# Kernel optimization log

Hardware: AMD Instinct MI355X
Metric: run time of the kernel (lower is better)

## Reference

```python
import jax, jax.numpy as jnp
import numpy as np

N_NODES = 100000
N_EDGES = 1600000
D = 128          # gnn_input_size == gnn_hidden_size
N_LAYERS = 7
N_GRAPHS = 64
N_CLASSES = 10
SNN_IN, SNN_H = 512, 1024
SNN_BETA = 0.85


def setup_inputs() -> dict:
    key = jax.random.key(0)
    ks = jax.random.split(key, 16)
    s = 0.05  # keep activations tame through 7 relu layers
    return {
        "snn_x": jax.random.normal(ks[0], (N_GRAPHS, SNN_IN), jnp.float32),
        "x": jax.random.normal(ks[1], (N_NODES, D), jnp.float32),
        "edge_index": jax.random.randint(ks[2], (2, N_EDGES), 0, N_NODES, jnp.int64),
        "batch": jnp.sort(jax.random.randint(ks[3], (N_NODES,), 0, N_GRAPHS, jnp.int64)),
        "snn_w1": jax.random.normal(ks[4], (SNN_IN, SNN_H), jnp.float32) * s,
        "snn_b1": jax.random.normal(ks[5], (SNN_H,), jnp.float32) * s,
        "snn_w2": jax.random.normal(ks[6], (SNN_H, N_CLASSES), jnp.float32) * s,
        "snn_b2": jax.random.normal(ks[7], (N_CLASSES,), jnp.float32) * s,
        "conv_wrel": jax.random.normal(ks[8], (N_LAYERS, D, D), jnp.float32) * s,
        "conv_wroot": jax.random.normal(ks[9], (N_LAYERS, D, D), jnp.float32) * s,
        "conv_brel": jax.random.normal(ks[10], (N_LAYERS, D), jnp.float32) * s,
        "lin_w": jax.random.normal(ks[11], (D, N_CLASSES), jnp.float32) * s,
        "lin_b": jax.random.normal(ks[12], (N_CLASSES,), jnp.float32) * s,
        "fuse_w": jax.random.normal(ks[13], (2 * N_CLASSES, N_CLASSES), jnp.float32) * s,
        "fuse_b": jax.random.normal(ks[14], (N_CLASSES,), jnp.float32) * s,
    }


def reference(snn_x, x, edge_index, batch,
              snn_w1, snn_b1, snn_w2, snn_b2,
              conv_wrel, conv_wroot, conv_brel,
              lin_w, lin_b, fuse_w, fuse_b):
    n = x.shape[0]
    src, dst = edge_index[0], edge_index[1]
    h = x
    for i in range(conv_wrel.shape[0]):
        agg = jax.ops.segment_sum(h[src], dst, num_segments=n)  # gather + scatter-add
        h = jax.nn.relu(agg @ conv_wrel[i] + conv_brel[i] + h @ conv_wroot[i])
    # global_mean_pool over batch segments
    sums = jax.ops.segment_sum(h, batch, num_segments=N_GRAPHS)
    cnts = jax.ops.segment_sum(jnp.ones((n,), h.dtype), batch, num_segments=N_GRAPHS)
    pooled = sums / jnp.maximum(cnts, 1.0)[:, None]
    gnn_logits = pooled @ lin_w + lin_b
    # SNN branch
    snn_h = jax.nn.relu(snn_x @ snn_w1 + snn_b1)
    snn_logits = SNN_BETA * (snn_h @ snn_w2 + snn_b2)
    # fusion
    fused = jnp.concatenate([snn_logits, gnn_logits], axis=-1)
    return fused @ fuse_w + fuse_b
```

## Files before the change

kernel.cpp:

```cpp
#include <hip/hip_runtime.h>
#include <hip/hip_bf16.h>

#define N_NODES 100000
#define N_EDGES 1600000
#define DIM     128
#define N_LAYERS 7
#define N_GRAPHS 64
#define SNN_IN  512
#define SNN_HID 1024
#define NCLS    10
#define M_PAD   100096
#define MBLK    782
#define NBK     782
#define SORT_CHUNK 4096
#define SORT_NCH   391
#define XPAIRS  (N_NODES * 64)
#define HPAIRS  (M_PAD * 64)
#define WELEMS  (N_LAYERS * DIM * 256)
#define AGG_BLOCKS 2048
#define AGG_WAVES  (AGG_BLOCKS * 4)
#define NQUAD   (N_NODES / 4)
#define POOL_NB 782
#define SS_PAD  2000384

typedef __attribute__((ext_vector_type(8))) short short8;
typedef __attribute__((ext_vector_type(4))) float f32x4;

__device__ __forceinline__ unsigned int f2bf(float f) {
    unsigned int u = __float_as_uint(f);
    return (u + 0x7fffu + ((u >> 16) & 1u)) >> 16;
}
__device__ __forceinline__ float bf2f(unsigned short b) {
    return __uint_as_float(((unsigned int)b) << 16);
}
__device__ __forceinline__ void acc_pair(unsigned int u, float& lo, float& hi) {
    lo += __uint_as_float(u << 16);
    hi += __uint_as_float(u & 0xffff0000u);
}

__global__ void k_convert(const float* __restrict__ x, const float* __restrict__ wrel,
                          const float* __restrict__ wroot, unsigned int* __restrict__ h,
                          unsigned short* __restrict__ Wt,
                          float* __restrict__ pooled, int* __restrict__ counts) {
    int i = blockIdx.x * blockDim.x + threadIdx.x;
    if (i < N_GRAPHS * 128) pooled[i] = 0.f;
    if (i >= N_GRAPHS * 128 && i < N_GRAPHS * 129) counts[i - N_GRAPHS * 128] = 0;
    if (i < XPAIRS) {
        float2 v = ((const float2*)x)[i];
        h[i] = f2bf(v.x) | (f2bf(v.y) << 16);
    } else if (i < HPAIRS) {
        h[i] = 0u;
    } else {
        int idx = i - HPAIRS;
        if (idx < WELEMS) {
            int l = idx >> 15, rem = idx & 32767, n = rem >> 8, k = rem & 255;
            float v = (k < 128) ? wrel[l * 16384 + k * 128 + n]
                                : wroot[l * 16384 + (k - 128) * 128 + n];
            Wt[idx] = (unsigned short)f2bf(v);
        }
    }
}

__global__ __launch_bounds__(256) void k_histA(const int* __restrict__ dst,
                                               int* __restrict__ chunk_hist) {
    __shared__ int hist[NBK];
    int b = blockIdx.x, t = threadIdx.x;
    int e0 = b * SORT_CHUNK;
    int e1 = e0 + SORT_CHUNK; if (e1 > N_EDGES) e1 = N_EDGES;
    for (int i = t; i < NBK; i += 256) hist[i] = 0;
    __syncthreads();
    for (int e = e0 + t; e < e1; e += 256) atomicAdd(&hist[dst[e] >> 7], 1);
    __syncthreads();
    for (int i = t; i < NBK; i += 256) chunk_hist[b * NBK + i] = hist[i];
}

__global__ __launch_bounds__(64) void k_colscan(int* __restrict__ chunk_hist,
                                                int* __restrict__ btot) {
    int b = blockIdx.x;
    int lane = threadIdx.x;
    const int C = (SORT_NCH + 63) / 64;
    int vals[C]; int sum = 0;
    #pragma unroll
    for (int j = 0; j < C; j++) {
        int c = lane * C + j;
        vals[j] = (c < SORT_NCH) ? chunk_hist[c * NBK + b] : 0;
        sum += vals[j];
    }
    int s = sum;
    #pragma unroll
    for (int o = 1; o < 64; o <<= 1) { int t = __shfl_up(s, o); if (lane >= o) s += t; }
    if (lane == 63) btot[b] = s;
    int run = s - sum;
    #pragma unroll
    for (int j = 0; j < C; j++) {
        int c = lane * C + j;
        if (c < SORT_NCH) chunk_hist[c * NBK + b] = run;
        run += vals[j];
    }
}

__global__ __launch_bounds__(256) void k_bscan(const int* __restrict__ btot,
                                               int* __restrict__ bucket_base) {
    __shared__ int wsum[4];
    int tid = threadIdx.x, lane = tid & 63, wid = tid >> 6;
    int i0 = tid * 4;
    int v[4]; int sum = 0;
    #pragma unroll
    for (int j = 0; j < 4; j++) { int i = i0 + j; v[j] = (i < NBK) ? btot[i] : 0; sum += v[j]; }
    int s = sum;
    #pragma unroll
    for (int o = 1; o < 64; o <<= 1) { int t = __shfl_up(s, o); if (lane >= o) s += t; }
    if (lane == 63) wsum[wid] = s;
    __syncthreads();
    if (tid == 0) {
        int acc = 0;
        #pragma unroll
        for (int w = 0; w < 4; w++) { acc += wsum[w]; wsum[w] = acc; }
    }
    __syncthreads();
    int prefix = s - sum + (wid ? wsum[wid - 1] : 0);
    #pragma unroll
    for (int j = 0; j < 4; j++) { int i = i0 + j; if (i < NBK) bucket_base[i] = prefix; prefix += v[j]; }
}

__global__ __launch_bounds__(256) void k_scatterA(const int* __restrict__ src,
                                                  const int* __restrict__ dst,
                                                  const int* __restrict__ chunk_hist,
                                                  const int* __restrict__ bucket_base,
                                                  unsigned int* __restrict__ pairs) {
    __shared__ int lcur[NBK];
    int b = blockIdx.x, t = threadIdx.x;
    int e0 = b * SORT_CHUNK;
    int e1 = e0 + SORT_CHUNK; if (e1 > N_EDGES) e1 = N_EDGES;
    for (int i = t; i < NBK; i += 256) lcur[i] = chunk_hist[b * NBK + i] + bucket_base[i];
    __syncthreads();
    for (int e = e0 + t; e < e1; e += 256) {
        int d = dst[e];
        int bk = d >> 7;
        int pos = atomicAdd(&lcur[bk], 1);
        pairs[pos] = (unsigned int)src[e] | ((unsigned int)(d & 127) << 17);
    }
}

__global__ __launch_bounds__(256) void k_bucketB(const unsigned int* __restrict__ pairs,
                                                 const int* __restrict__ bucket_base,
                                                 const int* __restrict__ btot,
                                                 int* __restrict__ row_off,
                                                 int* __restrict__ ndeg,
                                                 int* __restrict__ sorted_src) {
    __shared__ int lcnt[128];
    __shared__ int loff[128];
    int b = blockIdx.x, t = threadIdx.x;
    int node0 = b << 7;
    int nn = N_NODES - node0; if (nn > 128) nn = 128;
    int base = bucket_base[b];
    int end  = base + btot[b];
    int pbase = ((base + 3) & ~3) + 512 * b;
    if (t < 128) lcnt[t] = 0;
    __syncthreads();
    for (int i = base + t; i < end; i += 256) atomicAdd(&lcnt[pairs[i] >> 17], 1);
    __syncthreads();
    if (t < 64) {
        int v0 = (lcnt[2 * t] + 3) & ~3, v1 = (lcnt[2 * t + 1] + 3) & ~3;
        int s = v0 + v1, ps = s;
        #pragma unroll
        for (int o = 1; o < 64; o <<= 1) { int u = __shfl_up(ps, o); if (t >= o) ps += u; }
        int excl = ps - s;
        loff[2 * t] = excl; loff[2 * t + 1] = excl + v0;
    }
    __syncthreads();
    if (t < nn) {
        int d = lcnt[t];
        row_off[node0 + t] = pbase + loff[t];
        ndeg[node0 + t] = d;
        int pad = (d + 3) & ~3;
        for (int k = d; k < pad; k++) sorted_src[pbase + loff[t] + k] = N_NODES;
    }
    __syncthreads();
    if (t < 128) lcnt[t] = 0;
    __syncthreads();
    for (int i = base + t; i < end; i += 256) {
        unsigned int p = pairs[i];
        int l = p >> 17;
        int pos = atomicAdd(&lcnt[l], 1);
        sorted_src[pbase + loff[l] + pos] = (int)(p & 0x1FFFFu);
    }
}

#define GATH(d0, d1, d2, d3, s) \
    d0 = *(const uint4*)(hbl + (size_t)(((unsigned)(s).x) << 8)); \
    d1 = *(const uint4*)(hbl + (size_t)(((unsigned)(s).y) << 8)); \
    d2 = *(const uint4*)(hbl + (size_t)(((unsigned)(s).z) << 8)); \
    d3 = *(const uint4*)(hbl + (size_t)(((unsigned)(s).w) << 8));
#define ACC4(r0, r1, r2, r3) \
    acc_pair((r0).x, a[0], a[1]); acc_pair((r0).y, a[2], a[3]); \
    acc_pair((r0).z, a[4], a[5]); acc_pair((r0).w, a[6], a[7]); \
    acc_pair((r1).x, a[0], a[1]); acc_pair((r1).y, a[2], a[3]); \
    acc_pair((r1).z, a[4], a[5]); acc_pair((r1).w, a[6], a[7]); \
    acc_pair((r2).x, a[0], a[1]); acc_pair((r2).y, a[2], a[3]); \
    acc_pair((r2).z, a[4], a[5]); acc_pair((r2).w, a[6], a[7]); \
    acc_pair((r3).x, a[0], a[1]); acc_pair((r3).y, a[2], a[3]); \
    acc_pair((r3).z, a[4], a[5]); acc_pair((r3).w, a[6], a[7]);

__global__ __launch_bounds__(256) void k_agg(const char* __restrict__ hb,
                                             const int* __restrict__ row_off,
                                             const int* __restrict__ ndeg,
                                             const int4* __restrict__ sorted4,
                                             uint4* __restrict__ agg4) {
    int gw = blockIdx.x * 4 + (threadIdx.x >> 6);
    int lane = threadIdx.x & 63;
    int sub = lane >> 4, li = lane & 15;
    const char* hbl = hb + li * 16;
    for (int quad = gw; quad < NQUAD; quad += AGG_WAVES) {
        int node = quad * 4 + sub;
        int beg = row_off[node] >> 2;
        int nit = (ndeg[node] + 3) >> 2;
        float a[8] = {0.f, 0.f, 0.f, 0.f, 0.f, 0.f, 0.f, 0.f};
        if (nit > 0) {
            int4 sa = sorted4[beg];
            int4 sb = sorted4[beg + 1];
            uint4 A0, A1, A2, A3, B0, B1, B2, B3;
            GATH(A0, A1, A2, A3, sa);
            int it = 0;
            for (; it + 2 < nit; it += 2) {
                GATH(B0, B1, B2, B3, sb);
                sa = sorted4[beg + it + 2];
                ACC4(A0, A1, A2, A3);
                GATH(A0, A1, A2, A3, sa);
                sb = sorted4[beg + it + 3];
                ACC4(B0, B1, B2, B3);
            }
            if (it + 1 < nit) {
                GATH(B0, B1, B2, B3, sb);
                ACC4(A0, A1, A2, A3);
                ACC4(B0, B1, B2, B3);
            } else {
                ACC4(A0, A1, A2, A3);
            }
        }
        uint4 o;
        o.x = f2bf(a[0]) | (f2bf(a[1]) << 16);
        o.y = f2bf(a[2]) | (f2bf(a[3]) << 16);
        o.z = f2bf(a[4]) | (f2bf(a[5]) << 16);
        o.w = f2bf(a[6]) | (f2bf(a[7]) << 16);
        agg4[(size_t)node * 16 + li] = o;
    }
}

__global__ __launch_bounds__(256) void k_gemm(const unsigned short* __restrict__ Ag,
                                              const unsigned short* __restrict__ H,
                                              const unsigned short* __restrict__ Wt,
                                              const float* __restrict__ bias,
                                              unsigned short* __restrict__ Hout) {
    __shared__ unsigned short Es[64 * 144];
    int tid = threadIdx.x;
    int lane = tid & 63, wid = tid >> 6;
    int wr = (wid >> 1) * 64, wc = (wid & 1) * 64;
    int row0 = blockIdx.x * 128;
    f32x4 acc[4][4] = {};

    int ksub = (lane >> 4) * 8;
    const unsigned short* Aga = Ag + (size_t)(row0 + wr + (lane & 15)) * 128 + ksub;
    const unsigned short* Ha  = H  + (size_t)(row0 + wr + (lane & 15)) * 128 + ksub;
    const unsigned short* Bb  = Wt + (size_t)(wc + (lane & 15)) * 256 + ksub;

    auto load_frags = [&](short8* a, short8* b, int s) {
        const unsigned short* ab = (s < 4 ? Aga : Ha) + (s & 3) * 32;
        #pragma unroll
        for (int mi = 0; mi < 4; mi++) a[mi] = *(const short8*)(ab + mi * 16 * 128);
        const unsigned short* bp = Bb + s * 32;
        #pragma unroll
        for (int ni = 0; ni < 4; ni++) b[ni] = *(const short8*)(bp + ni * 16 * 256);
    };
    auto do_mfma = [&](short8* a, short8* b) {
        #pragma unroll
        for (int mi = 0; mi < 4; mi++)
            #pragma unroll
            for (int ni = 0; ni < 4; ni++)
                acc[mi][ni] = __builtin_amdgcn_mfma_f32_16x16x32_bf16(a[mi], b[ni], acc[mi][ni], 0, 0, 0);
    };

    short8 a0[4], b0[4], a1[4], b1[4];
    load_frags(a0, b0, 0);
    #pragma unroll
    for (int s = 0; s < 8; s += 2) {
        load_frags(a1, b1, s + 1);
        do_mfma(a0, b0);
        if (s + 2 < 8) load_frags(a0, b0, s + 2);
        do_mfma(a1, b1);
    }

    int cb = wc + (lane & 15);
    int rs = (lane >> 4) * 4;
    #pragma unroll
    for (int p = 0; p < 2; ++p) {
        __syncthreads();
        if (wr == 64 * p) {
            #pragma unroll
            for (int ni = 0; ni < 4; ni++) {
                int col = cb + ni * 16;
                float bn = bias[col];
                #pragma unroll
                for (int mi = 0; mi < 4; mi++) {
                    int rloc = mi * 16 + rs;
                    #pragma unroll
                    for (int rr = 0; rr < 4; rr++) {
                        float v = acc[mi][ni][rr] + bn;
                        v = v > 0.f ? v : 0.f;
                        if (row0 + 64 * p + rloc + rr >= N_NODES) v = 0.f;
                        Es[(rloc + rr) * 144 + col] = (unsigned short)f2bf(v);
                    }
                }
            }
        }
        __syncthreads();
        int rloc = tid >> 2;
        int c4 = (tid & 3) * 4;
        uint4* gd = (uint4*)(Hout + (size_t)(row0 + 64 * p + rloc) * 128);
        const uint4* es = (const uint4*)(Es + (size_t)rloc * 144);
        #pragma unroll
        for (int j = 0; j < 4; j++) gd[c4 + j] = es[c4 + j];
    }
}

__global__ __launch_bounds__(256) void k_pool_snn(const unsigned short* __restrict__ h,
                                                  const int* __restrict__ batch,
                                                  float* __restrict__ pooled,
                                                  int* __restrict__ counts,
                                                  const float* __restrict__ x,
                                                  const float* __restrict__ w1,
                                                  const float* __restrict__ b1,
                                                  float* __restrict__ snn_out) {
    if (blockIdx.x < POOL_NB) {
        __shared__ int bsh[128];
        int start = blockIdx.x * 128;
        int t = threadIdx.x & 127;
        int half = threadIdx.x >> 7;
        if (half == 0) {
            int end = start + 128; if (end > N_NODES) end = N_NODES;
            int nn = end - start;
            if (t < nn) bsh[t] = batch[start + t];
        }
        __syncthreads();
        if (half == 1) {
            int end = start + 128; if (end > N_NODES) end = N_NODES;
            int nn = end - start;
            float acc = 0.f; int cur = -1, cnt = 0;
            for (int i = 0; i < nn; i++) {
                int g = bsh[i];
                if (g != cur) {
                    if (cur >= 0) { atomicAdd(&pooled[cur * 128 + t], acc); if (t == 0) atomicAdd(&counts[cur], cnt); }
                    cur = g; acc = 0.f; cnt = 0;
                }
                acc += bf2f(h[(size_t)(start + i) * 128 + t]);
                cnt++;
            }
            if (cur >= 0) { atomicAdd(&pooled[cur * 128 + t], acc); if (t == 0) atomicAdd(&counts[cur], cnt); }
        }
    } else {
        int m = blockIdx.x - POOL_NB;
        __shared__ float xs[SNN_IN];
        int tid = threadIdx.x;
        for (int i = tid; i < SNN_IN; i += 256) xs[i] = x[m * SNN_IN + i];
        __syncthreads();
        float a0 = 0.f, a1 = 0.f, a2 = 0.f, a3 = 0.f;
        for (int k = 0; k < SNN_IN; k++) {
            float xv = xs[k];
            const float* wr = w1 + (size_t)k * SNN_HID + tid;
            a0 += xv * wr[0]; a1 += xv * wr[256]; a2 += xv * wr[512]; a3 += xv * wr[768];
        }
        float v;
        v = a0 + b1[tid];       snn_out[m * SNN_HID + tid]       = v > 0.f ? v : 0.f;
        v = a1 + b1[tid + 256]; snn_out[m * SNN_HID + tid + 256] = v > 0.f ? v : 0.f;
        v = a2 + b1[tid + 512]; snn_out[m * SNN_HID + tid + 512] = v > 0.f ? v : 0.f;
        v = a3 + b1[tid + 768]; snn_out[m * SNN_HID + tid + 768] = v > 0.f ? v : 0.f;
    }
}

__global__ __launch_bounds__(64) void k_head(const float* __restrict__ pooled, const int* __restrict__ counts,
                                             const float* __restrict__ lin_w, const float* __restrict__ lin_b,
                                             const float* __restrict__ snn_h, const float* __restrict__ w2,
                                             const float* __restrict__ b2, const float* __restrict__ fuse_w,
                                             const float* __restrict__ fuse_b, float* __restrict__ out) {
    int m = blockIdx.x, lane = threadIdx.x;
    __shared__ float sm[20];
    float cnt = (float)(counts[m] > 0 ? counts[m] : 1);
    float p0 = pooled[m * 128 + lane] / cnt;
    float p1 = pooled[m * 128 + 64 + lane] / cnt;
    for (int c = 0; c < NCLS; c++) {
        float v = p0 * lin_w[lane * 10 + c] + p1 * lin_w[(lane + 64) * 10 + c];
        #pragma unroll
        for (int o = 32; o > 0; o >>= 1) v += __shfl_down(v, o);
        if (lane == 0) sm[10 + c] = v + lin_b[c];
    }
    for (int c = 0; c < NCLS; c++) {
        float v = 0.f;
        #pragma unroll
        for (int j = 0; j < 16; j++) {
            int k = lane + j * 64;
            v += snn_h[m * SNN_HID + k] * w2[k * 10 + c];
        }
        #pragma unroll
        for (int o = 32; o > 0; o >>= 1) v += __shfl_down(v, o);
        if (lane == 0) sm[c] = 0.85f * (v + b2[c]);
    }
    __syncthreads();
    if (lane < NCLS) {
        float o = fuse_b[lane];
        #pragma unroll
        for (int j = 0; j < 20; j++) o += sm[j] * fuse_w[j * 10 + lane];
        out[m * 10 + lane] = o;
    }
}

extern "C" void kernel_launch(void* const* d_in, const int* in_sizes, int n_in,
                              void* d_out, int out_size, void* d_ws, size_t ws_size,
                              hipStream_t stream) {
    const float* snn_x  = (const float*)d_in[0];
    const float* x      = (const float*)d_in[1];
    const int*   ei     = (const int*)d_in[2];
    const int*   batch  = (const int*)d_in[3];
    const float* w1     = (const float*)d_in[4];
    const float* b1     = (const float*)d_in[5];
    const float* w2     = (const float*)d_in[6];
    const float* b2     = (const float*)d_in[7];
    const float* wrel   = (const float*)d_in[8];
    const float* wroot  = (const float*)d_in[9];
    const float* brel   = (const float*)d_in[10];
    const float* lin_w  = (const float*)d_in[11];
    const float* lin_b  = (const float*)d_in[12];
    const float* fuse_w = (const float*)d_in[13];
    const float* fuse_b = (const float*)d_in[14];
    const int* srcv = ei;
    const int* dstv = ei + N_EDGES;

    char* ws = (char*)d_ws;
    size_t off = 0;
    auto alloc = [&](size_t b) { char* p = ws + off; off = (off + b + 255) & ~(size_t)255; return p; };
    unsigned short* h0   = (unsigned short*)alloc((size_t)M_PAD * 128 * 2);
    unsigned short* h1   = (unsigned short*)alloc((size_t)M_PAD * 128 * 2);
    unsigned short* agg  = (unsigned short*)alloc((size_t)M_PAD * 128 * 2);
    unsigned short* Wt   = (unsigned short*)alloc((size_t)N_LAYERS * 128 * 256 * 2);
    int* sorted_src = (int*)alloc((size_t)SS_PAD * 4 + 16);
    unsigned int* pairs = (unsigned int*)alloc((size_t)N_EDGES * 4);
    int* chunk_hist = (int*)alloc((size_t)SORT_NCH * NBK * 4);
    int* row_off    = (int*)alloc((size_t)(N_NODES + 1) * 4);
    int* ndeg       = (int*)alloc((size_t)N_NODES * 4);
    int* btot       = (int*)alloc((size_t)NBK * 4);
    int* bucket_base= (int*)alloc((size_t)NBK * 4);
    float* pooled   = (float*)alloc((size_t)N_GRAPHS * 128 * 4);
    int* counts     = (int*)alloc((size_t)N_GRAPHS * 4);
    float* snn_h    = (float*)alloc((size_t)N_GRAPHS * SNN_HID * 4);

    k_histA<<<SORT_NCH, 256, 0, stream>>>(dstv, chunk_hist);
    k_colscan<<<NBK, 64, 0, stream>>>(chunk_hist, btot);
    k_bscan<<<1, 256, 0, stream>>>(btot, bucket_base);
    k_scatterA<<<SORT_NCH, 256, 0, stream>>>(srcv, dstv, chunk_hist, bucket_base, pairs);
    k_bucketB<<<NBK, 256, 0, stream>>>(pairs, bucket_base, btot, row_off, ndeg, sorted_src);
    k_convert<<<(HPAIRS + WELEMS + 255) / 256, 256, 0, stream>>>(x, wrel, wroot, (unsigned int*)h0,
                                                                 Wt, pooled, counts);

    unsigned short* hc = h0;
    unsigned short* hn = h1;
    for (int l = 0; l < N_LAYERS; l++) {
        k_agg<<<AGG_BLOCKS, 256, 0, stream>>>((const char*)hc, row_off, ndeg,
                                              (const int4*)sorted_src, (uint4*)agg);
        k_gemm<<<MBLK, 256, 0, stream>>>(agg, hc, Wt + (size_t)l * 128 * 256, brel + l * 128, hn);
        unsigned short* t = hc; hc = hn; hn = t;
    }
    k_pool_snn<<<POOL_NB + N_GRAPHS, 256, 0, stream>>>(hc, batch, pooled, counts,
                                                       snn_x, w1, b1, snn_h);
    k_head<<<N_GRAPHS, 64, 0, stream>>>(pooled, counts, lin_w, lin_b, snn_h, w2, b2, fuse_w, fuse_b,
                                        (float*)d_out);
}
```

Before: 932.5 us.

## Sort nodes by degree so aggregation waves process similar-degree nodes

Adds a degree histogram, a reverse scan and a scatter pass that build a node permutation ordered by descending in-degree. The aggregation kernel now reads its node IDs through this permutation, so the four nodes that share a wave have similar neighbor counts. This is meant to cut idle lanes caused by degree imbalance inside a wave. In exchange it adds three small preprocessing kernels and an extra indirection, and it loses sequential locality on the row_off and ndeg reads and on the output writes.

New measurement: 1.226 ms. 1.31x slower.

```diff
diff --git a/kernel.cpp b/kernel.cpp
--- a/kernel.cpp
+++ b/kernel.cpp
@@ -22,6 +22,7 @@
 #define NQUAD   (N_NODES / 4)
 #define POOL_NB 782
 #define SS_PAD  2000384
+#define DEG_BINS 64
 
 typedef __attribute__((ext_vector_type(8))) short short8;
 typedef __attribute__((ext_vector_type(4))) float f32x4;
@@ -100,9 +101,11 @@
 }
 
 __global__ __launch_bounds__(256) void k_bscan(const int* __restrict__ btot,
-                                               int* __restrict__ bucket_base) {
+                                               int* __restrict__ bucket_base,
+                                               int* __restrict__ deg_hist) {
     __shared__ int wsum[4];
     int tid = threadIdx.x, lane = tid & 63, wid = tid >> 6;
+    if (tid < DEG_BINS) deg_hist[tid] = 0;
     int i0 = tid * 4;
     int v[4]; int sum = 0;
     #pragma unroll
@@ -187,6 +190,43 @@
     }
 }
 
+__global__ __launch_bounds__(256) void k_deghist(const int* __restrict__ ndeg,
+                                                 int* __restrict__ hist) {
+    __shared__ int lh[DEG_BINS];
+    int t = threadIdx.x;
+    if (t < DEG_BINS) lh[t] = 0;
+    __syncthreads();
+    int i = blockIdx.x * 256 + t;
+    if (i < N_NODES) {
+        int d = ndeg[i]; if (d > DEG_BINS - 1) d = DEG_BINS - 1;
+        atomicAdd(&lh[d], 1);
+    }
+    __syncthreads();
+    if (t < DEG_BINS && lh[t]) atomicAdd(&hist[t], lh[t]);
+}
+
+__global__ __launch_bounds__(64) void k_degscan(const int* __restrict__ hist,
+                                                int* __restrict__ cursor) {
+    int t = threadIdx.x;
+    int rd = DEG_BINS - 1 - t;
+    int v = hist[rd];
+    int s = v;
+    #pragma unroll
+    for (int o = 1; o < 64; o <<= 1) { int u = __shfl_up(s, o); if (t >= o) s += u; }
+    cursor[rd] = s - v;
+}
+
+__global__ __launch_bounds__(256) void k_degscatter(const int* __restrict__ ndeg,
+                                                    int* __restrict__ cursor,
+                                                    int* __restrict__ qnode) {
+    int i = blockIdx.x * 256 + threadIdx.x;
+    if (i < N_NODES) {
+        int d = ndeg[i]; if (d > DEG_BINS - 1) d = DEG_BINS - 1;
+        int pos = atomicAdd(&cursor[d], 1);
+        qnode[pos] = i;
+    }
+}
+
 #define GATH(d0, d1, d2, d3, s) \
     d0 = *(const uint4*)(hbl + (size_t)(((unsigned)(s).x) << 8)); \
     d1 = *(const uint4*)(hbl + (size_t)(((unsigned)(s).y) << 8)); \
@@ -206,13 +246,14 @@
                                              const int* __restrict__ row_off,
                                              const int* __restrict__ ndeg,
                                              const int4* __restrict__ sorted4,
+                                             const int* __restrict__ qnode,
                                              uint4* __restrict__ agg4) {
     int gw = blockIdx.x * 4 + (threadIdx.x >> 6);
     int lane = threadIdx.x & 63;
     int sub = lane >> 4, li = lane & 15;
     const char* hbl = hb + li * 16;
     for (int quad = gw; quad < NQUAD; quad += AGG_WAVES) {
-        int node = quad * 4 + sub;
+        int node = qnode[quad * 4 + sub];
         int beg = row_off[node] >> 2;
         int nit = (ndeg[node] + 3) >> 2;
         float a[8] = {0.f, 0.f, 0.f, 0.f, 0.f, 0.f, 0.f, 0.f};
@@ -446,6 +487,9 @@
     int* chunk_hist = (int*)alloc((size_t)SORT_NCH * NBK * 4);
     int* row_off    = (int*)alloc((size_t)(N_NODES + 1) * 4);
     int* ndeg       = (int*)alloc((size_t)N_NODES * 4);
+    int* qnode      = (int*)alloc((size_t)N_NODES * 4);
+    int* deg_hist   = (int*)alloc((size_t)DEG_BINS * 4);
+    int* deg_cursor = (int*)alloc((size_t)DEG_BINS * 4);
     int* btot       = (int*)alloc((size_t)NBK * 4);
     int* bucket_base= (int*)alloc((size_t)NBK * 4);
     float* pooled   = (float*)alloc((size_t)N_GRAPHS * 128 * 4);
@@ -454,9 +498,12 @@
 
     k_histA<<<SORT_NCH, 256, 0, stream>>>(dstv, chunk_hist);
     k_colscan<<<NBK, 64, 0, stream>>>(chunk_hist, btot);
-    k_bscan<<<1, 256, 0, stream>>>(btot, bucket_base);
+    k_bscan<<<1, 256, 0, stream>>>(btot, bucket_base, deg_hist);
     k_scatterA<<<SORT_NCH, 256, 0, stream>>>(srcv, dstv, chunk_hist, bucket_base, pairs);
     k_bucketB<<<NBK, 256, 0, stream>>>(pairs, bucket_base, btot, row_off, ndeg, sorted_src);
+    k_deghist<<<(N_NODES + 255) / 256, 256, 0, stream>>>(ndeg, deg_hist);
+    k_degscan<<<1, 64, 0, stream>>>(deg_hist, deg_cursor);
+    k_degscatter<<<(N_NODES + 255) / 256, 256, 0, stream>>>(ndeg, deg_cursor, qnode);
     k_convert<<<(HPAIRS + WELEMS + 255) / 256, 256, 0, stream>>>(x, wrel, wroot, (unsigned int*)h0,
                                                                  Wt, pooled, counts);
 
@@ -464,7 +511,7 @@
     unsigned short* hn = h1;
     for (int l = 0; l < N_LAYERS; l++) {
         k_agg<<<AGG_BLOCKS, 256, 0, stream>>>((const char*)hc, row_off, ndeg,
-                                              (const int4*)sorted_src, (uint4*)agg);
+                                              (const int4*)sorted_src, qnode, (uint4*)agg);
         k_gemm<<<MBLK, 256, 0, stream>>>(agg, hc, Wt + (size_t)l * 128 * 256, brel + l * 128, hn);
         unsigned short* t = hc; hc = hn; hn = t;
     }
```

## Fuse neighbor aggregation with GraphConv GEMM into one per-layer kernel

Applied to the files above, without the earlier changes.

Replaces the separate aggregation and GEMM kernels with one kernel per layer. Each wave gathers and sums the neighbor rows for 16 nodes in registers, packs the sums straight into MFMA A fragments, and overlaps the gather for the next 16-node group with the current group's matrix multiply. This removes the intermediate aggregate buffer's global write and read and one launch per layer. In exchange, each lane now walks a different node's edge list, so the gather loads are less coalesced and lanes diverge when node degrees differ. Output stores are also no longer staged through shared memory.

Measured after the change: 1.828 ms. +96.0%, slower.

```diff
diff --git a/kernel.cpp b/kernel.cpp
--- a/kernel.cpp
+++ b/kernel.cpp
@@ -17,14 +17,13 @@
 #define XPAIRS  (N_NODES * 64)
 #define HPAIRS  (M_PAD * 64)
 #define WELEMS  (N_LAYERS * DIM * 256)
-#define AGG_BLOCKS 2048
-#define AGG_WAVES  (AGG_BLOCKS * 4)
-#define NQUAD   (N_NODES / 4)
 #define POOL_NB 782
 #define SS_PAD  2000384
+#define NG_REAL 6250
 
 typedef __attribute__((ext_vector_type(8))) short short8;
 typedef __attribute__((ext_vector_type(4))) float f32x4;
+typedef __attribute__((ext_vector_type(4))) unsigned int u32x4;
 
 __device__ __forceinline__ unsigned int f2bf(float f) {
     unsigned int u = __float_as_uint(f);
@@ -187,139 +186,129 @@
     }
 }
 
-#define GATH(d0, d1, d2, d3, s) \
-    d0 = *(const uint4*)(hbl + (size_t)(((unsigned)(s).x) << 8)); \
-    d1 = *(const uint4*)(hbl + (size_t)(((unsigned)(s).y) << 8)); \
-    d2 = *(const uint4*)(hbl + (size_t)(((unsigned)(s).z) << 8)); \
-    d3 = *(const uint4*)(hbl + (size_t)(((unsigned)(s).w) << 8));
-#define ACC4(r0, r1, r2, r3) \
-    acc_pair((r0).x, a[0], a[1]); acc_pair((r0).y, a[2], a[3]); \
-    acc_pair((r0).z, a[4], a[5]); acc_pair((r0).w, a[6], a[7]); \
-    acc_pair((r1).x, a[0], a[1]); acc_pair((r1).y, a[2], a[3]); \
-    acc_pair((r1).z, a[4], a[5]); acc_pair((r1).w, a[6], a[7]); \
-    acc_pair((r2).x, a[0], a[1]); acc_pair((r2).y, a[2], a[3]); \
-    acc_pair((r2).z, a[4], a[5]); acc_pair((r2).w, a[6], a[7]); \
-    acc_pair((r3).x, a[0], a[1]); acc_pair((r3).y, a[2], a[3]); \
-    acc_pair((r3).z, a[4], a[5]); acc_pair((r3).w, a[6], a[7]);
-
-__global__ __launch_bounds__(256) void k_agg(const char* __restrict__ hb,
-                                             const int* __restrict__ row_off,
-                                             const int* __restrict__ ndeg,
-                                             const int4* __restrict__ sorted4,
-                                             uint4* __restrict__ agg4) {
-    int gw = blockIdx.x * 4 + (threadIdx.x >> 6);
-    int lane = threadIdx.x & 63;
-    int sub = lane >> 4, li = lane & 15;
-    const char* hbl = hb + li * 16;
-    for (int quad = gw; quad < NQUAD; quad += AGG_WAVES) {
-        int node = quad * 4 + sub;
-        int beg = row_off[node] >> 2;
-        int nit = (ndeg[node] + 3) >> 2;
-        float a[8] = {0.f, 0.f, 0.f, 0.f, 0.f, 0.f, 0.f, 0.f};
-        if (nit > 0) {
-            int4 sa = sorted4[beg];
-            int4 sb = sorted4[beg + 1];
+#define CONSUME(c0, c1, c2, c3) do { \
+    acc_pair((c0).x, ac[0],  ac[1]);  acc_pair((c0).y, ac[2],  ac[3]);  \
+    acc_pair((c0).z, ac[4],  ac[5]);  acc_pair((c0).w, ac[6],  ac[7]);  \
+    acc_pair((c1).x, ac[8],  ac[9]);  acc_pair((c1).y, ac[10], ac[11]); \
+    acc_pair((c1).z, ac[12], ac[13]); acc_pair((c1).w, ac[14], ac[15]); \
+    acc_pair((c2).x, ac[16], ac[17]); acc_pair((c2).y, ac[18], ac[19]); \
+    acc_pair((c2).z, ac[20], ac[21]); acc_pair((c2).w, ac[22], ac[23]); \
+    acc_pair((c3).x, ac[24], ac[25]); acc_pair((c3).y, ac[26], ac[27]); \
+    acc_pair((c3).z, ac[28], ac[29]); acc_pair((c3).w, ac[30], ac[31]); \
+} while (0)
+
+__global__ __launch_bounds__(256) void k_fused(const char* __restrict__ hb,
+                                               const int* __restrict__ row_off,
+                                               const int* __restrict__ ndeg,
+                                               const int* __restrict__ sorted_src,
+                                               const unsigned short* __restrict__ WtL,
+                                               const float* __restrict__ bias,
+                                               unsigned short* __restrict__ Hout) {
+    int tid = threadIdx.x, lane = tid & 63, wi = tid >> 6;
+    int l4 = lane & 15, hq = lane >> 4;
+    const char* hbl = hb + hq * 16;
+    const char* bb  = (const char*)WtL + 512 * l4 + 16 * hq;
+
+    int ga = blockIdx.x * 8 + wi * 2;
+    if (ga >= NG_REAL) return;
+    int gb = ga + 1;
+    bool hasB = gb < NG_REAL;
+
+    float ac[32];
+    int g_it = 0, g_nit = 0;
+    const int* g_ssp = sorted_src;
+
+    auto ginit = [&](int g) {
+        int node = (g << 4) + l4;
+        g_nit = ndeg[node];
+        g_ssp = sorted_src + row_off[node];
+        g_it = 0;
+        #pragma unroll
+        for (int i = 0; i < 32; i++) ac[i] = 0.f;
+    };
+
+    auto grest = [&]() {
+        while (__ballot(g_it < g_nit)) {
+            if (g_it < g_nit) {
+                int x = g_ssp[g_it];
+                const char* p = hbl + ((size_t)(unsigned)x << 8);
+                uint4 c0 = *(const uint4*)p;
+                uint4 c1 = *(const uint4*)(p + 64);
+                uint4 c2 = *(const uint4*)(p + 128);
+                uint4 c3 = *(const uint4*)(p + 192);
+                CONSUME(c0, c1, c2, c3);
+            }
+            g_it++;
+        }
+    };
+
+    short8 afr[4];
+    auto packfr = [&]() {
+        #pragma unroll
+        for (int c = 0; c < 4; c++) {
+            u32x4 t;
+            t[0] = f2bf(ac[8 * c + 0]) | (f2bf(ac[8 * c + 1]) << 16);
+            t[1] = f2bf(ac[8 * c + 2]) | (f2bf(ac[8 * c + 3]) << 16);
+            t[2] = f2bf(ac[8 * c + 4]) | (f2bf(ac[8 * c + 5]) << 16);
+            t[3] = f2bf(ac[8 * c + 6]) | (f2bf(ac[8 * c + 7]) << 16);
+            afr[c] = __builtin_bit_cast(short8, t);
+        }
+    };
+
+    auto ctile = [&](int crow) {
+        const char* hr = hb + (size_t)(crow + l4) * 256 + 16 * hq;
+        f32x4 acc4[8];
+        #pragma unroll
+        for (int ni = 0; ni < 8; ni++) acc4[ni] = (f32x4){0.f, 0.f, 0.f, 0.f};
+        #pragma unroll
+        for (int s = 0; s < 8; s++) {
+            bool v0 = g_it < g_nit, v1 = g_it + 1 < g_nit;
             uint4 A0, A1, A2, A3, B0, B1, B2, B3;
-            GATH(A0, A1, A2, A3, sa);
-            int it = 0;
-            for (; it + 2 < nit; it += 2) {
-                GATH(B0, B1, B2, B3, sb);
-                sa = sorted4[beg + it + 2];
-                ACC4(A0, A1, A2, A3);
-                GATH(A0, A1, A2, A3, sa);
-                sb = sorted4[beg + it + 3];
-                ACC4(B0, B1, B2, B3);
-            }
-            if (it + 1 < nit) {
-                GATH(B0, B1, B2, B3, sb);
-                ACC4(A0, A1, A2, A3);
-                ACC4(B0, B1, B2, B3);
-            } else {
-                ACC4(A0, A1, A2, A3);
-            }
-        }
-        uint4 o;
-        o.x = f2bf(a[0]) | (f2bf(a[1]) << 16);
-        o.y = f2bf(a[2]) | (f2bf(a[3]) << 16);
-        o.z = f2bf(a[4]) | (f2bf(a[5]) << 16);
-        o.w = f2bf(a[6]) | (f2bf(a[7]) << 16);
-        agg4[(size_t)node * 16 + li] = o;
-    }
-}
-
-__global__ __launch_bounds__(256) void k_gemm(const unsigned short* __restrict__ Ag,
-                                              const unsigned short* __restrict__ H,
-                                              const unsigned short* __restrict__ Wt,
-                                              const float* __restrict__ bias,
-                                              unsigned short* __restrict__ Hout) {
-    __shared__ unsigned short Es[64 * 144];
-    int tid = threadIdx.x;
-    int lane = tid & 63, wid = tid >> 6;
-    int wr = (wid >> 1) * 64, wc = (wid & 1) * 64;
-    int row0 = blockIdx.x * 128;
-    f32x4 acc[4][4] = {};
-
-    int ksub = (lane >> 4) * 8;
-    const unsigned short* Aga = Ag + (size_t)(row0 + wr + (lane & 15)) * 128 + ksub;
-    const unsigned short* Ha  = H  + (size_t)(row0 + wr + (lane & 15)) * 128 + ksub;
-    const unsigned short* Bb  = Wt + (size_t)(wc + (lane & 15)) * 256 + ksub;
-
-    auto load_frags = [&](short8* a, short8* b, int s) {
-        const unsigned short* ab = (s < 4 ? Aga : Ha) + (s & 3) * 32;
-        #pragma unroll
-        for (int mi = 0; mi < 4; mi++) a[mi] = *(const short8*)(ab + mi * 16 * 128);
-        const unsigned short* bp = Bb + s * 32;
-        #pragma unroll
-        for (int ni = 0; ni < 4; ni++) b[ni] = *(const short8*)(bp + ni * 16 * 256);
+            if (v0) {
+                int x = g_ssp[g_it];
+                const char* p = hbl + ((size_t)(unsigned)x << 8);
+                A0 = *(const uint4*)p;         A1 = *(const uint4*)(p + 64);
+                A2 = *(const uint4*)(p + 128); A3 = *(const uint4*)(p + 192);
+            }
+            if (v1) {
+                int x = g_ssp[g_it + 1];
+                const char* p = hbl + ((size_t)(unsigned)x << 8);
+                B0 = *(const uint4*)p;         B1 = *(const uint4*)(p + 64);
+                B2 = *(const uint4*)(p + 128); B3 = *(const uint4*)(p + 192);
+            }
+            g_it += 2;
+            short8 av = (s < 4) ? afr[s] : *(const short8*)(hr + 64 * (s - 4));
+            #pragma unroll
+            for (int ni = 0; ni < 8; ni++) {
+                short8 bv = *(const short8*)(bb + ni * 8192 + s * 64);
+                acc4[ni] = __builtin_amdgcn_mfma_f32_16x16x32_bf16(av, bv, acc4[ni], 0, 0, 0);
+            }
+            if (v0) CONSUME(A0, A1, A2, A3);
+            if (v1) CONSUME(B0, B1, B2, B3);
+        }
+        #pragma unroll
+        for (int ni = 0; ni < 8; ni++) {
+            float bn = bias[ni * 16 + l4];
+            #pragma unroll
+            for (int rr = 0; rr < 4; rr++) {
+                int row = crow + 4 * hq + rr;
+                float v = acc4[ni][rr] + bn;
+                v = v > 0.f ? v : 0.f;
+                Hout[(size_t)row * 128 + ni * 16 + l4] = (unsigned short)f2bf(v);
+            }
+        }
     };
-    auto do_mfma = [&](short8* a, short8* b) {
-        #pragma unroll
-        for (int mi = 0; mi < 4; mi++)
-            #pragma unroll
-            for (int ni = 0; ni < 4; ni++)
-                acc[mi][ni] = __builtin_amdgcn_mfma_f32_16x16x32_bf16(a[mi], b[ni], acc[mi][ni], 0, 0, 0);
-    };
-
-    short8 a0[4], b0[4], a1[4], b1[4];
-    load_frags(a0, b0, 0);
-    #pragma unroll
-    for (int s = 0; s < 8; s += 2) {
-        load_frags(a1, b1, s + 1);
-        do_mfma(a0, b0);
-        if (s + 2 < 8) load_frags(a0, b0, s + 2);
-        do_mfma(a1, b1);
-    }
-
-    int cb = wc + (lane & 15);
-    int rs = (lane >> 4) * 4;
-    #pragma unroll
-    for (int p = 0; p < 2; ++p) {
-        __syncthreads();
-        if (wr == 64 * p) {
-            #pragma unroll
-            for (int ni = 0; ni < 4; ni++) {
-                int col = cb + ni * 16;
-                float bn = bias[col];
-                #pragma unroll
-                for (int mi = 0; mi < 4; mi++) {
-                    int rloc = mi * 16 + rs;
-                    #pragma unroll
-                    for (int rr = 0; rr < 4; rr++) {
-                        float v = acc[mi][ni][rr] + bn;
-                        v = v > 0.f ? v : 0.f;
-                        if (row0 + 64 * p + rloc + rr >= N_NODES) v = 0.f;
-                        Es[(rloc + rr) * 144 + col] = (unsigned short)f2bf(v);
-                    }
-                }
-            }
-        }
-        __syncthreads();
-        int rloc = tid >> 2;
-        int c4 = (tid & 3) * 4;
-        uint4* gd = (uint4*)(Hout + (size_t)(row0 + 64 * p + rloc) * 128);
-        const uint4* es = (const uint4*)(Es + (size_t)rloc * 144);
-        #pragma unroll
-        for (int j = 0; j < 4; j++) gd[c4 + j] = es[c4 + j];
+
+    ginit(ga);
+    grest();
+    packfr();
+    if (hasB) ginit(gb); else { g_nit = 0; g_it = 0; }
+    ctile(ga << 4);
+    grest();
+    if (hasB) {
+        packfr();
+        g_nit = 0; g_it = 0;
+        ctile(gb << 4);
     }
 }
 
@@ -439,7 +428,6 @@
     auto alloc = [&](size_t b) { char* p = ws + off; off = (off + b + 255) & ~(size_t)255; return p; };
     unsigned short* h0   = (unsigned short*)alloc((size_t)M_PAD * 128 * 2);
     unsigned short* h1   = (unsigned short*)alloc((size_t)M_PAD * 128 * 2);
-    unsigned short* agg  = (unsigned short*)alloc((size_t)M_PAD * 128 * 2);
     unsigned short* Wt   = (unsigned short*)alloc((size_t)N_LAYERS * 128 * 256 * 2);
     int* sorted_src = (int*)alloc((size_t)SS_PAD * 4 + 16);
     unsigned int* pairs = (unsigned int*)alloc((size_t)N_EDGES * 4);
@@ -463,9 +451,8 @@
     unsigned short* hc = h0;
     unsigned short* hn = h1;
     for (int l = 0; l < N_LAYERS; l++) {
-        k_agg<<<AGG_BLOCKS, 256, 0, stream>>>((const char*)hc, row_off, ndeg,
-                                              (const int4*)sorted_src, (uint4*)agg);
-        k_gemm<<<MBLK, 256, 0, stream>>>(agg, hc, Wt + (size_t)l * 128 * 256, brel + l * 128, hn);
+        k_fused<<<MBLK, 256, 0, stream>>>((const char*)hc, row_off, ndeg, sorted_src,
+                                          Wt + (size_t)l * 128 * 256, brel + l * 128, hn);
         unsigned short* t = hc; hc = hn; hn = t;
     }
     k_pool_snn<<<POOL_NB + N_GRAPHS, 256, 0, stream>>>(hc, batch, pooled, counts,
```

## Stage GEMM A tiles through swizzled LDS with async global_load_lds double buffering

Applied to the files above, without the earlier changes.

The GEMM used to load A fragments (aggregated and root features) straight from global memory into registers, with each wave re-reading its rows. It now stages 128x64 A tiles into LDS with the async global_load_lds path, using an XOR swizzle and double buffering across four k-steps, then reads the fragments from LDS. B fragments still come straight from global memory. This should cut duplicate global traffic and overlap loads with MFMA work, at the cost of more block-wide barriers and 32KB of LDS per block, which may lower occupancy.

After: 865.3 us. 1.08x faster.

```diff
diff --git a/kernel.cpp b/kernel.cpp
--- a/kernel.cpp
+++ b/kernel.cpp
@@ -22,6 +22,9 @@
 #define NQUAD   (N_NODES / 4)
 #define POOL_NB 782
 #define SS_PAD  2000384
+
+#define AS1 __attribute__((address_space(1)))
+#define AS3 __attribute__((address_space(3)))
 
 typedef __attribute__((ext_vector_type(8))) short short8;
 typedef __attribute__((ext_vector_type(4))) float f32x4;
@@ -252,46 +255,67 @@
                                               const unsigned short* __restrict__ Wt,
                                               const float* __restrict__ bias,
                                               unsigned short* __restrict__ Hout) {
-    __shared__ unsigned short Es[64 * 144];
+    __shared__ char smem[32768];
     int tid = threadIdx.x;
     int lane = tid & 63, wid = tid >> 6;
     int wr = (wid >> 1) * 64, wc = (wid & 1) * 64;
     int row0 = blockIdx.x * 128;
+    int l4 = lane & 15, hq = lane >> 4;
     f32x4 acc[4][4] = {};
 
-    int ksub = (lane >> 4) * 8;
-    const unsigned short* Aga = Ag + (size_t)(row0 + wr + (lane & 15)) * 128 + ksub;
-    const unsigned short* Ha  = H  + (size_t)(row0 + wr + (lane & 15)) * 128 + ksub;
-    const unsigned short* Bb  = Wt + (size_t)(wc + (lane & 15)) * 256 + ksub;
-
-    auto load_frags = [&](short8* a, short8* b, int s) {
-        const unsigned short* ab = (s < 4 ? Aga : Ha) + (s & 3) * 32;
-        #pragma unroll
-        for (int mi = 0; mi < 4; mi++) a[mi] = *(const short8*)(ab + mi * 16 * 128);
-        const unsigned short* bp = Bb + s * 32;
-        #pragma unroll
-        for (int ni = 0; ni < 4; ni++) b[ni] = *(const short8*)(bp + ni * 16 * 256);
+    int srow = tid >> 3, scc = tid & 7;
+    const unsigned short* bb = Wt + (size_t)(wc + l4) * 256 + hq * 8;
+
+    auto stage = [&](int buf, int kt) {
+        const unsigned short* P = (kt < 2) ? Ag : H;
+        int kbase = (kt & 1) * 64;
+        #pragma unroll
+        for (int j = 0; j < 4; j++) {
+            int row = srow + j * 32;
+            int cc = scc ^ (row & 7);
+            const unsigned short* g = P + (size_t)(row0 + row) * 128 + kbase + cc * 8;
+            char* l = smem + buf * 16384 + (j * 256 + wid * 64) * 16;
+            __builtin_amdgcn_global_load_lds((const AS1 unsigned int*)g,
+                                             (AS3 unsigned int*)l, 16, 0, 0);
+        }
     };
-    auto do_mfma = [&](short8* a, short8* b) {
-        #pragma unroll
-        for (int mi = 0; mi < 4; mi++)
+
+    auto compute = [&](int buf, int kt) {
+        const char* base = smem + buf * 16384;
+        #pragma unroll
+        for (int s2 = 0; s2 < 2; s2++) {
+            int sg = kt * 2 + s2;
+            short8 a[4], b[4];
+            #pragma unroll
+            for (int mi = 0; mi < 4; mi++) {
+                int row = wr + l4 + mi * 16;
+                int ci = (s2 * 4 + hq) ^ (l4 & 7);
+                a[mi] = *(const short8*)(base + row * 128 + ci * 16);
+            }
             #pragma unroll
             for (int ni = 0; ni < 4; ni++)
-                acc[mi][ni] = __builtin_amdgcn_mfma_f32_16x16x32_bf16(a[mi], b[ni], acc[mi][ni], 0, 0, 0);
+                b[ni] = *(const short8*)(bb + (size_t)ni * 16 * 256 + sg * 32);
+            #pragma unroll
+            for (int mi = 0; mi < 4; mi++)
+                #pragma unroll
+                for (int ni = 0; ni < 4; ni++)
+                    acc[mi][ni] = __builtin_amdgcn_mfma_f32_16x16x32_bf16(a[mi], b[ni], acc[mi][ni], 0, 0, 0);
+        }
     };
 
-    short8 a0[4], b0[4], a1[4], b1[4];
-    load_frags(a0, b0, 0);
-    #pragma unroll
-    for (int s = 0; s < 8; s += 2) {
-        load_frags(a1, b1, s + 1);
-        do_mfma(a0, b0);
-        if (s + 2 < 8) load_frags(a0, b0, s + 2);
-        do_mfma(a1, b1);
-    }
-
-    int cb = wc + (lane & 15);
-    int rs = (lane >> 4) * 4;
+    stage(0, 0);
+    int cur = 0;
+    #pragma unroll
+    for (int kt = 0; kt < 4; kt++) {
+        __syncthreads();
+        if (kt < 3) stage(cur ^ 1, kt + 1);
+        compute(cur, kt);
+        cur ^= 1;
+    }
+
+    unsigned short* Es = (unsigned short*)smem;
+    int cb = wc + l4;
+    int rs = hq * 4;
     #pragma unroll
     for (int p = 0; p < 2; ++p) {
         __syncthreads();
```
